# Kernel tuning notes

Hardware: AMD Instinct MI355X
Metric: run time of the kernel (lower is better)

## Reference

```python
import jax, jax.numpy as jnp
import numpy as np

B, L, K1, P = 16, 224, 8192, 16  # batch, spectral bands, pixels, endmembers
LEAKY_SLOPE = 0.01  # torch nn.LeakyReLU default


def setup_inputs() -> dict:
    key = jax.random.key(0)
    ks = jax.random.split(key, 7)
    return {
        "a": jax.random.normal(ks[0], (B, P, K1), jnp.float32),
        "d2": jax.random.normal(ks[1], (B, P, K1), jnp.float32),
        "y": jax.random.normal(ks[2], (B, L, K1), jnp.float32),
        "w3_w": jax.random.normal(ks[3], (P, P), jnp.float32) * 0.1,  # Conv1d(P,P,1) weight squeezed
        "b3_w": jax.random.normal(ks[4], (P, P), jnp.float32) * 0.1,
        "w3_c": jax.random.normal(ks[5], (1, L, P), jnp.float32),     # kernel codebook
        "sigma": jnp.ones((1,), jnp.float32) * 2.0,
        "ca_w": jax.random.normal(ks[6], (2, P), jnp.float32) * 0.1,  # CA Conv1d(P,2,1) weight squeezed
    }


def reference(a, d2, y, w3_w, b3_w, w3_c, sigma, ca_w):
    # h2 = Conv1d(P,P,1)(a - d2)  -> pointwise matmul over channel dim
    h2 = jnp.einsum('pq,bqn->bpn', w3_w, a - d2)  # (B,P,K1)

    # GaussianKernelLayer: pairwise L2 distances between y pixels (B,L,K1)
    # and codebook columns w3_c (1,L,P), via the GEMM identity
    # ||u-v||^2 = ||u||^2 + ||v||^2 - 2 u.v  (avoids the (B,L,K1,P) broadcast).
    y_sq = jnp.sum(y * y, axis=1)            # (B,K1)
    c_sq = jnp.sum(w3_c * w3_c, axis=1)      # (1,P)
    cross = jnp.einsum('blk,olp->bkp', y, w3_c)  # (B,K1,P)
    dist_sq = jnp.maximum(y_sq[:, :, None] + c_sq[:, None, :] - 2.0 * cross, 0.0)
    dist = jnp.sqrt(dist_sq)                 # (B,K1,P)
    h3 = jnp.exp(-0.5 * jnp.square(dist / sigma[0]))
    h3 = jnp.transpose(h3, (0, 2, 1))        # (B,P,K1)

    # CA channel attention: avg/max pool over pixels -> Conv1d(P,2,1) -> LeakyReLU -> softmax
    avg = jnp.mean(h3, axis=-1)              # (B,P)
    mx = jnp.max(h3, axis=-1)                # (B,P)
    conv_lrelu = lambda v: jax.nn.leaky_relu(jnp.einsum('cp,bp->bc', ca_w, v), LEAKY_SLOPE)
    ratio = jax.nn.softmax(conv_lrelu(avg) + conv_lrelu(mx), axis=-1)  # (B,2)

    # combine center pixel + mean pixel via bmm with ratio
    mid = h3[:, :, K1 // 2]                  # (B,P)
    mean = jnp.mean(h3, axis=-1)             # (B,P)
    stacked = jnp.stack([mid, mean], axis=1)  # (B,2,P)
    comb = jnp.einsum('bc,bcp->bp', ratio, stacked)  # (B,P)

    # h4 = Conv1d(P,P,1)(comb[:, :, None])
    h4 = jnp.einsum('pq,bq->bp', b3_w, comb)[:, :, None]  # (B,P,1)

    return h4 + h2  # broadcast over pixel dim -> (B,P,K1)
```

## Files before the change

kernel.cpp:

```cpp
#include <hip/hip_runtime.h>

#define Bn  16
#define Ln  224
#define K1n 8192
#define Pn  16
#define NCHUNK 16
#define RG  16
#define NG  (Ln / RG)


__global__ __launch_bounds__(512, 2) void k_stats(
    const float* __restrict__ y,
    const float* __restrict__ w3c,
    const float* __restrict__ sigma,
    float* __restrict__ ws_sum,
    float* __restrict__ ws_max,
    float* __restrict__ ws_mid)
{
    __shared__ float s_csq_part[32][Pn];
    __shared__ float s_csq[Pn];
    __shared__ float s_part_s[8][Pn];
    __shared__ float s_part_m[8][Pn];

    const int tid   = threadIdx.x;
    const int lane  = tid & 63;
    const int wv    = tid >> 6;
    const int b     = blockIdx.x >> 4;
    const int chunk = blockIdx.x & 15;

    {
        const int p   = tid & 15;
        const int sub = tid >> 4;
        float cs = 0.f;
        for (int l = sub; l < Ln; l += 32) {
            float v = w3c[l * Pn + p];
            cs = fmaf(v, v, cs);
        }
        s_csq_part[sub][p] = cs;
    }
    __syncthreads();
    if (tid < Pn) {
        float cs = 0.f;
#pragma unroll
        for (int s = 0; s < 32; ++s) cs += s_csq_part[s][tid];
        s_csq[tid] = cs;
    }
    __syncthreads();

    float cross[Pn];
#pragma unroll
    for (int p = 0; p < Pn; ++p) cross[p] = 0.f;
    float ysq = 0.f;

    const float* yp = y + (size_t)b * Ln * K1n + (chunk << 9) + tid;

    float v[RG], vn[RG];
#pragma unroll
    for (int j = 0; j < RG; ++j)
        v[j] = __builtin_nontemporal_load(yp + (size_t)j * K1n);

    for (int g = 0; g < NG; ++g) {
        if (g < NG - 1) {
#pragma unroll
            for (int j = 0; j < RG; ++j)
                vn[j] = __builtin_nontemporal_load(
                            yp + (size_t)((g + 1) * RG + j) * K1n);
        }
        const float* wrow = w3c + (size_t)g * RG * Pn;
#pragma unroll
        for (int j = 0; j < RG; ++j) {
            ysq = fmaf(v[j], v[j], ysq);
#pragma unroll
            for (int p = 0; p < Pn; ++p)
                cross[p] = fmaf(v[j], wrow[j * Pn + p], cross[p]);
        }
        if (g < NG - 1) {
#pragma unroll
            for (int j = 0; j < RG; ++j) v[j] = vn[j];
        }
    }

    const float sg = sigma[0];
    const float nh = -0.5f / (sg * sg);

    float h3[Pn];
#pragma unroll
    for (int p = 0; p < Pn; ++p) {
        float d = fmaxf(ysq + s_csq[p] - 2.f * cross[p], 0.f);
        h3[p] = __expf(d * nh);
    }

    if (chunk == 8 && tid == 0) {
#pragma unroll
        for (int p = 0; p < Pn; ++p) ws_mid[b * Pn + p] = h3[p];
    }

#pragma unroll
    for (int p = 0; p < Pn; ++p) {
        float s = h3[p];
        float m = h3[p];
#pragma unroll
        for (int off = 32; off > 0; off >>= 1) {
            s += __shfl_down(s, off, 64);
            m = fmaxf(m, __shfl_down(m, off, 64));
        }
        if (lane == 0) { s_part_s[wv][p] = s; s_part_m[wv][p] = m; }
    }
    __syncthreads();
    if (tid < Pn) {
        float s = 0.f, m = -1.f;
#pragma unroll
        for (int w = 0; w < 8; ++w) {
            s += s_part_s[w][tid];
            m = fmaxf(m, s_part_m[w][tid]);
        }
        const int base = (b * NCHUNK + chunk) * Pn + tid;
        ws_sum[base] = s;
        ws_max[base] = m;
    }
}

__global__ __launch_bounds__(512, 2) void k_out(
    const float* __restrict__ a,
    const float* __restrict__ d2,
    const float* __restrict__ w3w,
    const float* __restrict__ b3w,
    const float* __restrict__ caw,
    const float* __restrict__ ws_sum,
    const float* __restrict__ ws_max,
    const float* __restrict__ ws_mid,
    float* __restrict__ out)
{
    __shared__ float s_red_s[16][Pn];
    __shared__ float s_red_m[16][Pn];
    __shared__ float s_avg[Pn], s_mx[Pn], s_mid[Pn], s_h4[Pn];
    __shared__ float s_t[2];

    const int tid = threadIdx.x;
    const int b   = blockIdx.x >> 4;
    const int kb  = (blockIdx.x & 15) << 9;

    const float* ap = a  + (size_t)b * Pn * K1n + kb + tid;
    const float* dp = d2 + (size_t)b * Pn * K1n + kb + tid;
    float av[Pn], dv[Pn];
#pragma unroll
    for (int q = 0; q < Pn; ++q) av[q] = ap[(size_t)q * K1n];
#pragma unroll
    for (int q = 0; q < Pn; ++q) dv[q] = dp[(size_t)q * K1n];

    if (tid < 256) {
        const int p   = tid & 15;
        const int grp = tid >> 4;
        const int i0  = (b * NCHUNK + grp) * Pn + p;
        s_red_s[grp][p] = ws_sum[i0];
        s_red_m[grp][p] = ws_max[i0];
    }
    __syncthreads();
    if (tid < Pn) {
        float s = 0.f, m = -1.f;
#pragma unroll
        for (int g = 0; g < 16; ++g) {
            s += s_red_s[g][tid];
            m = fmaxf(m, s_red_m[g][tid]);
        }
        s_avg[tid] = s * (1.f / (float)K1n);
        s_mx[tid]  = m;
        s_mid[tid] = ws_mid[b * Pn + tid];
    }
    __syncthreads();

    if (tid < 2) {
        float t1 = 0.f, t2 = 0.f;
        for (int p = 0; p < Pn; ++p) {
            float cw = caw[tid * Pn + p];
            t1 = fmaf(cw, s_avg[p], t1);
            t2 = fmaf(cw, s_mx[p],  t2);
        }
        t1 = (t1 > 0.f) ? t1 : 0.01f * t1;
        t2 = (t2 > 0.f) ? t2 : 0.01f * t2;
        s_t[tid] = t1 + t2;
    }
    __syncthreads();

    if (tid < Pn) {
        float t0 = s_t[0], u1 = s_t[1];
        float mt = fmaxf(t0, u1);
        float e0 = __expf(t0 - mt), e1 = __expf(u1 - mt);
        float inv = 1.f / (e0 + e1);
        s_red_s[0][tid] = (e0 * inv) * s_mid[tid] + (e1 * inv) * s_avg[tid];
    }
    __syncthreads();

    if (tid < Pn) {
        float h = 0.f;
        for (int q = 0; q < Pn; ++q) h = fmaf(b3w[tid * Pn + q], s_red_s[0][q], h);
        s_h4[tid] = h;
    }
    __syncthreads();

    float diff[Pn];
#pragma unroll
    for (int q = 0; q < Pn; ++q) diff[q] = av[q] - dv[q];

    float* op = out + (size_t)b * Pn * K1n + kb + tid;
#pragma unroll
    for (int p = 0; p < Pn; ++p) {
        float h2 = s_h4[p];
#pragma unroll
        for (int q = 0; q < Pn; ++q)
            h2 = fmaf(w3w[p * Pn + q], diff[q], h2);
        op[(size_t)p * K1n] = h2;
    }
}

extern "C" void kernel_launch(void* const* d_in, const int* in_sizes, int n_in,
                              void* d_out, int out_size, void* d_ws, size_t ws_size,
                              hipStream_t stream) {
    const float* a     = (const float*)d_in[0];
    const float* d2    = (const float*)d_in[1];
    const float* y     = (const float*)d_in[2];
    const float* w3w   = (const float*)d_in[3];
    const float* b3w   = (const float*)d_in[4];
    const float* w3c   = (const float*)d_in[5];
    const float* sigma = (const float*)d_in[6];
    const float* caw   = (const float*)d_in[7];

    float* ws_sum = (float*)d_ws;
    float* ws_max = ws_sum + Bn * NCHUNK * Pn;
    float* ws_mid = ws_max + Bn * NCHUNK * Pn;

    k_stats<<<dim3(Bn * NCHUNK), dim3(512), 0, stream>>>(
        y, w3c, sigma, ws_sum, ws_max, ws_mid);

    k_out<<<dim3(Bn * NCHUNK), dim3(512), 0, stream>>>(
        a, d2, w3w, b3w, caw, ws_sum, ws_max, ws_mid, (float*)d_out);
}
```

Before: 200.1 us.

## Split cross-product stage over band halves with two pixels per thread

The y·codebook cross product moves into a new kernel that splits the 224 bands into two halves and has each thread process two adjacent pixels with float2 loads. Partial cross sums and squared norms go to a workspace, and a second kernel combines the halves before computing h3 statistics. This changes grid shape and per-thread work to improve memory-level parallelism on the dominant y read. In exchange it adds a 16 MB round trip through the workspace for partial sums and one more kernel launch.

```diff
diff --git a/kernel.cpp b/kernel.cpp
--- a/kernel.cpp
+++ b/kernel.cpp
@@ -4,15 +4,88 @@
 #define Ln  224
 #define K1n 8192
 #define Pn  16
+#define LH  2
+#define LROWS 112
+#define KC  8
+#define RG  16
+#define NGc (LROWS / RG)
 #define NCHUNK 16
-#define RG  16
-#define NG  (Ln / RG)
-
-
-__global__ __launch_bounds__(512, 2) void k_stats(
+
+typedef float f2 __attribute__((ext_vector_type(2)));
+
+
+__global__ __launch_bounds__(512, 2) void k_cross(
     const float* __restrict__ y,
     const float* __restrict__ w3c,
+    float* __restrict__ wsC,
+    float* __restrict__ wsY)
+{
+    const int tid = threadIdx.x;
+    const int b   = blockIdx.x >> 4;
+    const int lh  = (blockIdx.x >> 3) & 1;
+    const int kc  = blockIdx.x & 7;
+
+    float cross0[Pn], cross1[Pn];
+#pragma unroll
+    for (int p = 0; p < Pn; ++p) { cross0[p] = 0.f; cross1[p] = 0.f; }
+    float ysq0 = 0.f, ysq1 = 0.f;
+
+    const float* ybase = y + (size_t)b * Ln * K1n
+                           + (size_t)lh * LROWS * K1n + (kc << 10);
+    const f2* yp = reinterpret_cast<const f2*>(ybase) + tid;
+
+    f2 v[RG], vn[RG];
+#pragma unroll
+    for (int j = 0; j < RG; ++j)
+        v[j] = __builtin_nontemporal_load(yp + (size_t)j * (K1n / 2));
+
+    for (int g = 0; g < NGc; ++g) {
+        if (g < NGc - 1) {
+#pragma unroll
+            for (int j = 0; j < RG; ++j)
+                vn[j] = __builtin_nontemporal_load(
+                            yp + (size_t)((g + 1) * RG + j) * (K1n / 2));
+        }
+        const float* wrow = w3c + (size_t)(lh * LROWS + g * RG) * Pn;
+#pragma unroll
+        for (int j = 0; j < RG; ++j) {
+            ysq0 = fmaf(v[j].x, v[j].x, ysq0);
+            ysq1 = fmaf(v[j].y, v[j].y, ysq1);
+#pragma unroll
+            for (int p = 0; p < Pn; ++p) {
+                const float w = wrow[j * Pn + p];
+                cross0[p] = fmaf(v[j].x, w, cross0[p]);
+                cross1[p] = fmaf(v[j].y, w, cross1[p]);
+            }
+        }
+        if (g < NGc - 1) {
+#pragma unroll
+            for (int j = 0; j < RG; ++j) v[j] = vn[j];
+        }
+    }
+
+    const size_t kk = (size_t)(kc << 10) + 2 * tid;
+    float4* wc4 = reinterpret_cast<float4*>(
+        wsC + ((size_t)(b * LH + lh) * K1n + kk) * Pn);
+    wc4[0] = make_float4(cross0[0],  cross0[1],  cross0[2],  cross0[3]);
+    wc4[1] = make_float4(cross0[4],  cross0[5],  cross0[6],  cross0[7]);
+    wc4[2] = make_float4(cross0[8],  cross0[9],  cross0[10], cross0[11]);
+    wc4[3] = make_float4(cross0[12], cross0[13], cross0[14], cross0[15]);
+    wc4[4] = make_float4(cross1[0],  cross1[1],  cross1[2],  cross1[3]);
+    wc4[5] = make_float4(cross1[4],  cross1[5],  cross1[6],  cross1[7]);
+    wc4[6] = make_float4(cross1[8],  cross1[9],  cross1[10], cross1[11]);
+    wc4[7] = make_float4(cross1[12], cross1[13], cross1[14], cross1[15]);
+
+    float2* wy2 = reinterpret_cast<float2*>(
+        wsY + (size_t)(b * LH + lh) * K1n + kk);
+    *wy2 = make_float2(ysq0, ysq1);
+}
+
+__global__ __launch_bounds__(512, 2) void k_h3(
+    const float* __restrict__ w3c,
     const float* __restrict__ sigma,
+    const float* __restrict__ wsC,
+    const float* __restrict__ wsY,
     float* __restrict__ ws_sum,
     float* __restrict__ ws_max,
     float* __restrict__ ws_mid)
@@ -27,6 +100,7 @@
     const int wv    = tid >> 6;
     const int b     = blockIdx.x >> 4;
     const int chunk = blockIdx.x & 15;
+    const int k     = (chunk << 9) + tid;
 
     {
         const int p   = tid & 15;
@@ -47,38 +121,21 @@
     }
     __syncthreads();
 
-    float cross[Pn];
-#pragma unroll
-    for (int p = 0; p < Pn; ++p) cross[p] = 0.f;
-    float ysq = 0.f;
-
-    const float* yp = y + (size_t)b * Ln * K1n + (chunk << 9) + tid;
-
-    float v[RG], vn[RG];
-#pragma unroll
-    for (int j = 0; j < RG; ++j)
-        v[j] = __builtin_nontemporal_load(yp + (size_t)j * K1n);
-
-    for (int g = 0; g < NG; ++g) {
-        if (g < NG - 1) {
-#pragma unroll
-            for (int j = 0; j < RG; ++j)
-                vn[j] = __builtin_nontemporal_load(
-                            yp + (size_t)((g + 1) * RG + j) * K1n);
-        }
-        const float* wrow = w3c + (size_t)g * RG * Pn;
-#pragma unroll
-        for (int j = 0; j < RG; ++j) {
-            ysq = fmaf(v[j], v[j], ysq);
-#pragma unroll
-            for (int p = 0; p < Pn; ++p)
-                cross[p] = fmaf(v[j], wrow[j * Pn + p], cross[p]);
-        }
-        if (g < NG - 1) {
-#pragma unroll
-            for (int j = 0; j < RG; ++j) v[j] = vn[j];
-        }
-    }
+    const float4* q0 = reinterpret_cast<const float4*>(
+        wsC + ((size_t)(b * LH + 0) * K1n + k) * Pn);
+    const float4* q1 = reinterpret_cast<const float4*>(
+        wsC + ((size_t)(b * LH + 1) * K1n + k) * Pn);
+    float4 t0 = q0[0], t1 = q0[1], t2 = q0[2], t3 = q0[3];
+    float4 u0 = q1[0], u1 = q1[1], u2 = q1[2], u3 = q1[3];
+
+    float cr[Pn];
+    cr[0]  = t0.x + u0.x; cr[1]  = t0.y + u0.y; cr[2]  = t0.z + u0.z; cr[3]  = t0.w + u0.w;
+    cr[4]  = t1.x + u1.x; cr[5]  = t1.y + u1.y; cr[6]  = t1.z + u1.z; cr[7]  = t1.w + u1.w;
+    cr[8]  = t2.x + u2.x; cr[9]  = t2.y + u2.y; cr[10] = t2.z + u2.z; cr[11] = t2.w + u2.w;
+    cr[12] = t3.x + u3.x; cr[13] = t3.y + u3.y; cr[14] = t3.z + u3.z; cr[15] = t3.w + u3.w;
+
+    const float ysq = wsY[(size_t)(b * LH + 0) * K1n + k]
+                    + wsY[(size_t)(b * LH + 1) * K1n + k];
 
     const float sg = sigma[0];
     const float nh = -0.5f / (sg * sg);
@@ -86,7 +143,7 @@
     float h3[Pn];
 #pragma unroll
     for (int p = 0; p < Pn; ++p) {
-        float d = fmaxf(ysq + s_csq[p] - 2.f * cross[p], 0.f);
+        float d = fmaxf(ysq + s_csq[p] - 2.f * cr[p], 0.f);
         h3[p] = __expf(d * nh);
     }
 
@@ -131,8 +188,8 @@
     const float* __restrict__ ws_mid,
     float* __restrict__ out)
 {
-    __shared__ float s_red_s[16][Pn];
-    __shared__ float s_red_m[16][Pn];
+    __shared__ float s_red_s[NCHUNK][Pn];
+    __shared__ float s_red_m[NCHUNK][Pn];
     __shared__ float s_avg[Pn], s_mx[Pn], s_mid[Pn], s_h4[Pn];
     __shared__ float s_t[2];
 
@@ -159,7 +216,7 @@
     if (tid < Pn) {
         float s = 0.f, m = -1.f;
 #pragma unroll
-        for (int g = 0; g < 16; ++g) {
+        for (int g = 0; g < NCHUNK; ++g) {
             s += s_red_s[g][tid];
             m = fmaxf(m, s_red_m[g][tid]);
         }
@@ -225,12 +282,17 @@
     const float* sigma = (const float*)d_in[6];
     const float* caw   = (const float*)d_in[7];
 
-    float* ws_sum = (float*)d_ws;
+    float* wsC    = (float*)d_ws;
+    float* wsY    = wsC + (size_t)Bn * LH * K1n * Pn;
+    float* ws_sum = wsY + (size_t)Bn * LH * K1n;
     float* ws_max = ws_sum + Bn * NCHUNK * Pn;
     float* ws_mid = ws_max + Bn * NCHUNK * Pn;
 
-    k_stats<<<dim3(Bn * NCHUNK), dim3(512), 0, stream>>>(
-        y, w3c, sigma, ws_sum, ws_max, ws_mid);
+    k_cross<<<dim3(Bn * LH * KC), dim3(512), 0, stream>>>(
+        y, w3c, wsC, wsY);
+
+    k_h3<<<dim3(Bn * NCHUNK), dim3(512), 0, stream>>>(
+        w3c, sigma, wsC, wsY, ws_sum, ws_max, ws_mid);
 
     k_out<<<dim3(Bn * NCHUNK), dim3(512), 0, stream>>>(
         a, d2, w3w, b3w, caw, ws_sum, ws_max, ws_mid, (float*)d_out);
```

Measured after the change: 229.6 us. +14.7%, slower.
